# Optimization experiments

Hardware: AMD Instinct MI355X
Metric: run time of the kernel (lower is better)

## Reference

```python
import jax, jax.numpy as jnp
import numpy as np

DIM = 128
N = 16          # num_nodes
B = 8           # batch size
H = 4096        # MLP hidden width
SLOPE = 0.01    # LeakyReLU default negative slope
PI_ITERS = 50   # fixed-iteration power iteration (max_error=1e-5 regime)


def setup_inputs() -> dict:
    key = jax.random.key(0)
    ks = jax.random.split(key, 12)
    w = lambda k, shape: jax.random.normal(k, shape, jnp.float32) * 0.02
    return {
        "nodes_embeddings": jax.random.normal(ks[0], (B, N, DIM), jnp.float32),
        "graphs_embeddings": jax.random.normal(ks[1], (B, DIM), jnp.float32),
        "Ts": jax.random.uniform(ks[2], (B, N, N), jnp.float32),
        "W1": w(ks[3], (2 * DIM, H)), "b1": jnp.zeros((H,), jnp.float32),
        "W2": w(ks[4], (H, H)),       "b2": jnp.zeros((H,), jnp.float32),
        "W3": w(ks[5], (H, H)),       "b3": jnp.zeros((H,), jnp.float32),
        "W4": w(ks[6], (H, N * N)),   "b4": jnp.zeros((N * N,), jnp.float32),
    }


def _mlp(x, W1, b1, W2, b2, W3, b3, W4, b4):
    # Linear -> LeakyReLU -> (Dropout=eval identity), x3, then Linear -> LeakyReLU -> Sigmoid
    h = jax.nn.leaky_relu(x @ W1 + b1, SLOPE)
    h = jax.nn.leaky_relu(h @ W2 + b2, SLOPE)
    h = jax.nn.leaky_relu(h @ W3 + b3, SLOPE)
    return jax.nn.sigmoid(jax.nn.leaky_relu(h @ W4 + b4, SLOPE))


def _power_iteration(A):
    # A: (..., n, n), entries > 0 (sigmoid outputs) -> dominant (Perron) eigenvector.
    v0 = jnp.ones(A.shape[:-1], A.dtype)
    def step(v, _):
        w = jnp.einsum('...ij,...j->...i', A, v)
        v = w / jnp.linalg.norm(w, axis=-1, keepdims=True)
        return v, None
    v, _ = jax.lax.scan(step, v0, None, length=PI_ITERS)
    return v


def reference(nodes_embeddings, graphs_embeddings, Ts, W1, b1, W2, b2, W3, b3, W4, b4):
    Bn, Nn, D = nodes_embeddings.shape
    P = Nn * Nn
    pair = jnp.arange(P)
    s_ids = pair // Nn  # outer loop index s
    t_ids = pair % Nn   # inner loop index t

    embT = jnp.transpose(nodes_embeddings, (1, 0, 2))      # (N, B, D)
    s_all = embT[s_ids]                                    # (P, B, D)
    t_all = embT[t_ids]                                    # (P, B, D)
    # Faithful to torch.stack([s, t]).view(batch, 2*dim): a flat reinterpretation,
    # NOT a per-row concat. stack axis=1 -> (P, 2, B, D) then reshape -> (P, B, 2D).
    x = jnp.stack([s_all, t_all], axis=1).reshape(P, Bn, 2 * D)

    pol = _mlp(x.reshape(P * Bn, 2 * D), W1, b1, W2, b2, W3, b3, W4, b4)
    pol = pol.reshape(P, Bn, Nn, Nn)                       # predecessor prob matrices

    vec = _power_iteration(pol)                            # (P, B, N)
    v_src = vec[pair, :, s_ids]                            # (P, B) eigenvector[src]
    T_pair = jnp.transpose(Ts.reshape(Bn, P), (1, 0))      # (P, B), pair order s*N+t

    contrib = vec / v_src[:, :, None] * T_pair[:, :, None]  # (P, B, N)
    return jnp.sum(contrib, axis=0)                         # (B, N) == Cs
```

## Files before the change

kernel.cpp:

```cpp
#include <hip/hip_runtime.h>

typedef unsigned short u16;
typedef unsigned int u32;
typedef __attribute__((ext_vector_type(8))) short short8;
typedef __attribute__((ext_vector_type(4))) float f32x4;

__device__ __forceinline__ u16 f2bf(float f) {
    unsigned u = __float_as_uint(f);
    return (u16)((u + 0x7FFFu + ((u >> 16) & 1u)) >> 16);
}
__device__ __forceinline__ u32 pack2(float a, float b) {
    return ((u32)f2bf(b) << 16) | (u32)f2bf(a);
}
__device__ __forceinline__ float bf2f(u16 w) { return __uint_as_float((u32)w << 16); }

#define ROR1 0x121
#define ROR2 0x122
#define ROR4 0x124
#define ROR8 0x128
template<int C> __device__ __forceinline__ float dppf(float x) {
    int i = __float_as_int(x);
    return __int_as_float(__builtin_amdgcn_update_dpp(i, i, C, 0xF, 0xF, false));
}
template<int C> __device__ __forceinline__ int dppi(int x) {
    return __builtin_amdgcn_update_dpp(x, x, C, 0xF, 0xF, false);
}

template<int SRC, int EPI>
__global__ __launch_bounds__(256, 2) void k_gemm(
    const u16* __restrict__ A, const float* __restrict__ emb,
    const float* __restrict__ W, const float* __restrict__ bias,
    u16* __restrict__ Cp16, u16* __restrict__ Ho,
    int N, int kchunk)
{
    __shared__ __align__(16) u16 Alds[64][40];
    __shared__ __align__(16) u32 Wlds[16 * 132];
    int tid = threadIdx.x;
    int wv = tid >> 6, lane = tid & 63, c = lane & 15, g = lane >> 4;
    int c0 = blockIdx.x * 128;
    int k0 = blockIdx.y * kchunk;
    int nit = kchunk >> 5;

    int ar = tid >> 2, aseg = tid & 3;
    int kp = tid >> 4, cbase = (tid & 15) * 8;

    f32x4 acc[8];
    #pragma unroll
    for (int n = 0; n < 8; ++n) acc[n] = (f32x4){0.f, 0.f, 0.f, 0.f};

    auto loadA = [&](int kc, uint4& av) {
        if (SRC == 0) {
            av = *(const uint4*)(A + (size_t)ar * 4096 + k0 + kc + aseg * 8);
        } else {
            int e0 = kc + aseg * 8;
            int b = 2 * (ar & 3) + (e0 >> 7), d = e0 & 127;
            const float4* s = (const float4*)(emb + (b * 16 + (ar >> 2)) * 128 + d);
            float4 f0 = s[0], f1 = s[1];
            av.x = pack2(f0.x, f0.y); av.y = pack2(f0.z, f0.w);
            av.z = pack2(f1.x, f1.y); av.w = pack2(f1.z, f1.w);
        }
    };
    auto loadW = [&](int kc, float4& q0, float4& q1, float4& q2, float4& q3) {
        const float* s0 = W + (size_t)(k0 + kc + 2 * kp) * N + c0 + cbase;
        q0 = ((const float4*)s0)[0]; q1 = ((const float4*)s0)[1];
        const float* s1 = s0 + N;
        q2 = ((const float4*)s1)[0]; q3 = ((const float4*)s1)[1];
    };
    auto stage = [&](const uint4& av, const float4& q0, const float4& q1,
                     const float4& q2, const float4& q3) {
        *(uint4*)&Alds[ar][aseg * 8] = av;
        uint4 w0, w1;
        w0.x = pack2(q0.x, q2.x); w0.y = pack2(q0.y, q2.y);
        w0.z = pack2(q0.z, q2.z); w0.w = pack2(q0.w, q2.w);
        w1.x = pack2(q1.x, q3.x); w1.y = pack2(q1.y, q3.y);
        w1.z = pack2(q1.z, q3.z); w1.w = pack2(q1.w, q3.w);
        uint4* wd = (uint4*)&Wlds[kp * 132 + cbase];
        wd[0] = w0; wd[1] = w1;
    };
    auto compute = [&]() {
        short8 a8 = *(const short8*)&Alds[wv * 16 + c][g * 8];
        #pragma unroll
        for (int n = 0; n < 8; ++n) {
            int base = n * 16 + c;
            union { u32 u[4]; short8 s; } bb;
            bb.u[0] = Wlds[(g * 4 + 0) * 132 + base];
            bb.u[1] = Wlds[(g * 4 + 1) * 132 + base];
            bb.u[2] = Wlds[(g * 4 + 2) * 132 + base];
            bb.u[3] = Wlds[(g * 4 + 3) * 132 + base];
            acc[n] = __builtin_amdgcn_mfma_f32_16x16x32_bf16(a8, bb.s, acc[n], 0, 0, 0);
        }
    };

    uint4 avA, avB;
    float4 qA0, qA1, qA2, qA3, qB0, qB1, qB2, qB3;
    loadA(0, avA);  loadW(0, qA0, qA1, qA2, qA3);
    loadA(32, avB); loadW(32, qB0, qB1, qB2, qB3);

    for (int it = 0; it < nit; it += 2) {
        stage(avA, qA0, qA1, qA2, qA3);
        __syncthreads();
        if (it + 2 < nit) { loadA((it + 2) * 32, avA); loadW((it + 2) * 32, qA0, qA1, qA2, qA3); }
        compute();
        __syncthreads();

        stage(avB, qB0, qB1, qB2, qB3);
        __syncthreads();
        if (it + 3 < nit) { loadA((it + 3) * 32, avB); loadW((it + 3) * 32, qB0, qB1, qB2, qB3); }
        compute();
        __syncthreads();
    }

    #pragma unroll
    for (int n = 0; n < 8; ++n) {
        #pragma unroll
        for (int rr = 0; rr < 4; ++rr) {
            int grow = wv * 16 + g * 4 + rr;
            int gcol = c0 + n * 16 + c;
            float v = acc[n][rr];
            if (EPI == 0) {
                Cp16[(size_t)blockIdx.y * 64 * N + (size_t)grow * N + gcol] = f2bf(v);
            } else {
                v += bias[gcol];
                v = (v >= 0.f) ? v : 0.01f * v;
                Ho[(size_t)grow * N + gcol] = f2bf(v);
            }
        }
    }
}

__global__ void k_reduce(const u16* __restrict__ Cp16, const float* __restrict__ bias,
                         u16* __restrict__ Hb, float* __restrict__ Pf,
                         int N, int ksplit, int mode)
{
    int idx = blockIdx.x * 256 + threadIdx.x;
    int col = idx & (N - 1);
    float s = bias[col];
    #pragma unroll 4
    for (int k = 0; k < ksplit; ++k) s += bf2f(Cp16[(size_t)k * 64 * N + idx]);
    float a = (s >= 0.f) ? s : 0.01f * s;
    if (mode == 0) Hb[idx] = f2bf(a);
    else           Pf[idx] = 1.0f / (1.0f + __expf(-a));
}

__global__ __launch_bounds__(1024) void k_power_out(
    const float* __restrict__ pol,
    const float* __restrict__ Ts,
    float* __restrict__ out)
{
    __shared__ float pol_lds[16384];
    __shared__ float w_lds[64][16];
    __shared__ float Ts_lds[2048];
    __shared__ float Cmat[8][16];

    int tid = threadIdx.x;
    int m = tid >> 4, r = tid & 15;

    {
        const float4* p4 = (const float4*)(pol + tid * 16);
        float4* q4 = (float4*)&pol_lds[tid * 16];
        q4[0] = p4[0]; q4[1] = p4[1]; q4[2] = p4[2]; q4[3] = p4[3];
    }
    Ts_lds[tid] = Ts[tid];
    Ts_lds[tid + 1024] = Ts[tid + 1024];
    __syncthreads();

    float Mr[8], Ms[8];
    {
        int mb = m * 256 + r * 16;
        int idx = r;
        #pragma unroll
        for (int k = 0; k < 8; ++k) { Mr[k] = pol_lds[mb + idx]; idx = dppi<ROR1>(idx); }
        #pragma unroll
        for (int k = 0; k < 8; ++k) { Ms[k] = pol_lds[mb + idx]; idx = dppi<ROR1>(idx); }
    }

    float v = 1.0f;
    #pragma unroll 1
    for (int it = 0; it < 50; ++it) {
        float va = v, vb = dppf<ROR8>(v);
        float w = 0.f, w2 = 0.f;
        #pragma unroll
        for (int k = 0; k < 8; ++k) {
            w  = fmaf(Mr[k], va, w);
            w2 = fmaf(Ms[k], vb, w2);
            if (k < 7) { va = dppf<ROR1>(va); vb = dppf<ROR1>(vb); }
        }
        w += w2;
        if ((it & 7) == 7) {
            float s = w;
            s += dppf<ROR8>(s); s += dppf<ROR4>(s);
            s += dppf<ROR2>(s); s += dppf<ROR1>(s);
            w *= 1.0f / s;
        }
        v = w;
    }
    w_lds[m][r] = v;
    __syncthreads();

    if (tid < 128) {
        int b = tid >> 4, x = tid & 15;
        float s = 0.f;
        if (b < 4) {
            const float* row = &Ts_lds[(b * 16 + x) * 16];
            #pragma unroll
            for (int t = 0; t < 16; ++t) s += row[t];
        } else {
            int j = b - 4;
            #pragma unroll
            for (int si = 0; si < 16; ++si)
                s += Ts_lds[(b * 16 + si) * 16 + x] / w_lds[x * 4 + j][si];
        }
        Cmat[b][x] = s;
    }
    __syncthreads();

    if (tid < 128) {
        int b = tid >> 4, n = tid & 15;
        float o = 0.f;
        if (b < 4) {
            #pragma unroll
            for (int si = 0; si < 16; ++si) {
                const float* wr = w_lds[si * 4 + b];
                o += wr[n] / wr[si] * Cmat[b][si];
            }
        } else {
            int j = b - 4;
            #pragma unroll
            for (int t = 0; t < 16; ++t)
                o += w_lds[t * 4 + j][n] * Cmat[b][t];
        }
        out[b * 16 + n] = o;
    }
}

extern "C" void kernel_launch(void* const* d_in, const int* in_sizes, int n_in,
                              void* d_out, int out_size, void* d_ws, size_t ws_size,
                              hipStream_t stream)
{
    const float* emb = (const float*)d_in[0];
    const float* Ts  = (const float*)d_in[2];
    const float* W1  = (const float*)d_in[3];  const float* b1 = (const float*)d_in[4];
    const float* W2  = (const float*)d_in[5];  const float* b2 = (const float*)d_in[6];
    const float* W3  = (const float*)d_in[7];  const float* b3 = (const float*)d_in[8];
    const float* W4  = (const float*)d_in[9];  const float* b4 = (const float*)d_in[10];
    float* outp = (float*)d_out;

    char* ws = (char*)d_ws;
    u16*   Ha  = (u16*)(ws + 0);
    u16*   Hb  = (u16*)(ws + 524288);
    float* pol = (float*)(ws + 1048576);
    u16*   Cp  = (u16*)(ws + 1114112);

    size_t need16 = (size_t)1114112 + (size_t)16 * 524288;
    int KS = (ws_size >= need16) ? 16 : 8;
    int kchunk = 4096 / KS;

    k_gemm<1, 1><<<dim3(32, 1), 256, 0, stream>>>(
        nullptr, emb, W1, b1, nullptr, Ha, 4096, 256);

    k_gemm<0, 0><<<dim3(32, KS), 256, 0, stream>>>(
        Ha, nullptr, W2, nullptr, Cp, nullptr, 4096, kchunk);
    k_reduce<<<1024, 256, 0, stream>>>(Cp, b2, Hb, nullptr, 4096, KS, 0);

    k_gemm<0, 0><<<dim3(32, KS), 256, 0, stream>>>(
        Hb, nullptr, W3, nullptr, Cp, nullptr, 4096, kchunk);
    k_reduce<<<1024, 256, 0, stream>>>(Cp, b3, Ha, nullptr, 4096, KS, 0);

    k_gemm<0, 0><<<dim3(2, 32), 256, 0, stream>>>(
        Ha, nullptr, W4, nullptr, Cp, nullptr, 256, 128);
    k_reduce<<<64, 256, 0, stream>>>(Cp, b4, nullptr, pol, 256, 32, 1);

    k_power_out<<<1, 1024, 0, stream>>>(pol, Ts, outp);

    (void)in_sizes; (void)n_in; (void)out_size; (void)ws_size;
}
```

Baseline: 75.51 us.

## Deepen GEMM prefetch to four stages and fuse final reduce into power kernel

The GEMM main loop now keeps four K-slices of A and W loads in flight in registers instead of two, to hide more global-memory latency. The last split-K reduce with bias, LeakyReLU and sigmoid is folded into the power-iteration kernel, removing one launch and the fp32 pol round trip through global memory. The extra prefetch registers may push pressure past the launch bound. The fused reduce also runs inside a single-block kernel, so its 32-way summation is serialised per thread.

```diff
diff --git a/kernel.cpp b/kernel.cpp
--- a/kernel.cpp
+++ b/kernel.cpp
@@ -13,6 +13,8 @@
     return ((u32)f2bf(b) << 16) | (u32)f2bf(a);
 }
 __device__ __forceinline__ float bf2f(u16 w) { return __uint_as_float((u32)w << 16); }
+__device__ __forceinline__ float bfhi(u32 w) { return __uint_as_float(w & 0xFFFF0000u); }
+__device__ __forceinline__ float bflo(u32 w) { return __uint_as_float(w << 16); }
 
 #define ROR1 0x121
 #define ROR2 0x122
@@ -91,21 +93,36 @@
         }
     };
 
-    uint4 avA, avB;
-    float4 qA0, qA1, qA2, qA3, qB0, qB1, qB2, qB3;
-    loadA(0, avA);  loadW(0, qA0, qA1, qA2, qA3);
-    loadA(32, avB); loadW(32, qB0, qB1, qB2, qB3);
-
-    for (int it = 0; it < nit; it += 2) {
-        stage(avA, qA0, qA1, qA2, qA3);
-        __syncthreads();
-        if (it + 2 < nit) { loadA((it + 2) * 32, avA); loadW((it + 2) * 32, qA0, qA1, qA2, qA3); }
+    uint4 av0, av1, av2, av3;
+    float4 q00, q01, q02, q03, q10, q11, q12, q13;
+    float4 q20, q21, q22, q23, q30, q31, q32, q33;
+    loadA(0,  av0); loadW(0,  q00, q01, q02, q03);
+    loadA(32, av1); loadW(32, q10, q11, q12, q13);
+    loadA(64, av2); loadW(64, q20, q21, q22, q23);
+    loadA(96, av3); loadW(96, q30, q31, q32, q33);
+
+    for (int it = 0; it < nit; it += 4) {
+        stage(av0, q00, q01, q02, q03);
+        __syncthreads();
+        if (it + 4 < nit) { loadA((it + 4) * 32, av0); loadW((it + 4) * 32, q00, q01, q02, q03); }
         compute();
         __syncthreads();
 
-        stage(avB, qB0, qB1, qB2, qB3);
-        __syncthreads();
-        if (it + 3 < nit) { loadA((it + 3) * 32, avB); loadW((it + 3) * 32, qB0, qB1, qB2, qB3); }
+        stage(av1, q10, q11, q12, q13);
+        __syncthreads();
+        if (it + 5 < nit) { loadA((it + 5) * 32, av1); loadW((it + 5) * 32, q10, q11, q12, q13); }
+        compute();
+        __syncthreads();
+
+        stage(av2, q20, q21, q22, q23);
+        __syncthreads();
+        if (it + 6 < nit) { loadA((it + 6) * 32, av2); loadW((it + 6) * 32, q20, q21, q22, q23); }
+        compute();
+        __syncthreads();
+
+        stage(av3, q30, q31, q32, q33);
+        __syncthreads();
+        if (it + 7 < nit) { loadA((it + 7) * 32, av3); loadW((it + 7) * 32, q30, q31, q32, q33); }
         compute();
         __syncthreads();
     }
@@ -129,8 +146,7 @@
 }
 
 __global__ void k_reduce(const u16* __restrict__ Cp16, const float* __restrict__ bias,
-                         u16* __restrict__ Hb, float* __restrict__ Pf,
-                         int N, int ksplit, int mode)
+                         u16* __restrict__ Hb, int N, int ksplit)
 {
     int idx = blockIdx.x * 256 + threadIdx.x;
     int col = idx & (N - 1);
@@ -138,12 +154,12 @@
     #pragma unroll 4
     for (int k = 0; k < ksplit; ++k) s += bf2f(Cp16[(size_t)k * 64 * N + idx]);
     float a = (s >= 0.f) ? s : 0.01f * s;
-    if (mode == 0) Hb[idx] = f2bf(a);
-    else           Pf[idx] = 1.0f / (1.0f + __expf(-a));
+    Hb[idx] = f2bf(a);
 }
 
 __global__ __launch_bounds__(1024) void k_power_out(
-    const float* __restrict__ pol,
+    const u16* __restrict__ Cp16,
+    const float* __restrict__ bias,
     const float* __restrict__ Ts,
     float* __restrict__ out)
 {
@@ -156,9 +172,29 @@
     int m = tid >> 4, r = tid & 15;
 
     {
-        const float4* p4 = (const float4*)(pol + tid * 16);
-        float4* q4 = (float4*)&pol_lds[tid * 16];
-        q4[0] = p4[0]; q4[1] = p4[1]; q4[2] = p4[2]; q4[3] = p4[3];
+        int e0 = tid * 16;
+        float s[16];
+        #pragma unroll
+        for (int j = 0; j < 16; ++j) s[j] = 0.f;
+        for (int k = 0; k < 32; ++k) {
+            const uint4* q = (const uint4*)(Cp16 + (size_t)k * 16384 + e0);
+            uint4 w0 = q[0], w1 = q[1];
+            s[0]  += bflo(w0.x); s[1]  += bfhi(w0.x);
+            s[2]  += bflo(w0.y); s[3]  += bfhi(w0.y);
+            s[4]  += bflo(w0.z); s[5]  += bfhi(w0.z);
+            s[6]  += bflo(w0.w); s[7]  += bfhi(w0.w);
+            s[8]  += bflo(w1.x); s[9]  += bfhi(w1.x);
+            s[10] += bflo(w1.y); s[11] += bfhi(w1.y);
+            s[12] += bflo(w1.z); s[13] += bfhi(w1.z);
+            s[14] += bflo(w1.w); s[15] += bfhi(w1.w);
+        }
+        int colb = e0 & 255;
+        #pragma unroll
+        for (int j = 0; j < 16; ++j) {
+            float a = s[j] + bias[colb + j];
+            a = (a >= 0.f) ? a : 0.01f * a;
+            pol_lds[e0 + j] = 1.0f / (1.0f + __expf(-a));
+        }
     }
     Ts_lds[tid] = Ts[tid];
     Ts_lds[tid + 1024] = Ts[tid + 1024];
@@ -248,10 +284,9 @@
     char* ws = (char*)d_ws;
     u16*   Ha  = (u16*)(ws + 0);
     u16*   Hb  = (u16*)(ws + 524288);
-    float* pol = (float*)(ws + 1048576);
-    u16*   Cp  = (u16*)(ws + 1114112);
-
-    size_t need16 = (size_t)1114112 + (size_t)16 * 524288;
+    u16*   Cp  = (u16*)(ws + 1048576);
+
+    size_t need16 = (size_t)1048576 + (size_t)16 * 524288;
     int KS = (ws_size >= need16) ? 16 : 8;
     int kchunk = 4096 / KS;
 
@@ -260,17 +295,16 @@
 
     k_gemm<0, 0><<<dim3(32, KS), 256, 0, stream>>>(
         Ha, nullptr, W2, nullptr, Cp, nullptr, 4096, kchunk);
-    k_reduce<<<1024, 256, 0, stream>>>(Cp, b2, Hb, nullptr, 4096, KS, 0);
+    k_reduce<<<1024, 256, 0, stream>>>(Cp, b2, Hb, 4096, KS);
 
     k_gemm<0, 0><<<dim3(32, KS), 256, 0, stream>>>(
         Hb, nullptr, W3, nullptr, Cp, nullptr, 4096, kchunk);
-    k_reduce<<<1024, 256, 0, stream>>>(Cp, b3, Ha, nullptr, 4096, KS, 0);
+    k_reduce<<<1024, 256, 0, stream>>>(Cp, b3, Ha, 4096, KS);
 
     k_gemm<0, 0><<<dim3(2, 32), 256, 0, stream>>>(
         Ha, nullptr, W4, nullptr, Cp, nullptr, 256, 128);
-    k_reduce<<<64, 256, 0, stream>>>(Cp, b4, nullptr, pol, 256, 32, 1);
-
-    k_power_out<<<1, 1024, 0, stream>>>(pol, Ts, outp);
+
+    k_power_out<<<1, 1024, 0, stream>>>(Cp, b4, Ts, outp);
 
     (void)in_sizes; (void)n_in; (void)out_size; (void)ws_size;
 }
```

Result: slower. 85.55 us (+13.3%).
